# Optimization experiments

Measured on AMD Instinct MI355X. Metric: run time of the kernel, lower is better.

Reference implementation:

```python
import jax, jax.numpy as jnp
import numpy as np

H = 4   # num_attention_heads
C = 32  # attention_head_size
LN_EPS = 1e-5

def setup_inputs() -> dict:
    key = jax.random.key(0)
    ks = jax.random.split(key, 8)
    E = 128  # embedding_channels; all_head_size = H*C = 128
    B, I, J = 1, 256, 256
    s = 1.0 / np.sqrt(E)
    return {
        "z": jax.random.normal(ks[0], (B, I, J, E), dtype=jnp.float32),
        "ln_scale": jnp.ones((E,), jnp.float32),
        "ln_bias": jnp.zeros((E,), jnp.float32),
        # weights stored as [in, out] (torch Linear applies x @ W.T; here y = x @ W)
        "Wq": jax.random.normal(ks[1], (E, H * C), jnp.float32) * s,
        "Wk": jax.random.normal(ks[2], (E, H * C), jnp.float32) * s,
        "Wv": jax.random.normal(ks[3], (E, H * C), jnp.float32) * s,
        "Wg": jax.random.normal(ks[4], (E, H * C), jnp.float32) * s,
        "bg": jnp.zeros((H * C,), jnp.float32),
        "Wo": jax.random.normal(ks[5], (H * C, E), jnp.float32) * s,
        "bo": jnp.zeros((E,), jnp.float32),
    }

def reference(z, ln_scale, ln_bias, Wq, Wk, Wv, Wg, bg, Wo, bo):
    B, I, J, E = z.shape
    # LayerNorm over last dim
    mu = jnp.mean(z, axis=-1, keepdims=True)
    var = jnp.mean(jnp.square(z - mu), axis=-1, keepdims=True)
    zn = (z - mu) * jax.lax.rsqrt(var + LN_EPS) * ln_scale + ln_bias
    # QKV projections, reshaped to heads: [B, I, J, H, C]
    q = (zn @ Wq).reshape(B, I, J, H, C)
    k = (zn @ Wk).reshape(B, I, J, H, C)
    v = (zn @ Wv).reshape(B, I, J, H, C)
    # Row-wise attention (NOTE: original has no 1/sqrt(c) scaling)
    logits = jnp.einsum('biqhc,bikhc->bihqk', q, k)  # [B, I, H, J, J]
    weights = jax.nn.softmax(logits, axis=-1)
    wavg = jnp.einsum('bihqk,bikhc->biqhc', weights, v)  # [B, I, J, H, C]
    # Sigmoid gate
    g = jax.nn.sigmoid((zn @ Wg + bg).reshape(B, I, J, H, C))
    out = (g * wavg).reshape(B, I, J, H * C)
    return out @ Wo + bo
```

## Files before the change

### kernel.cpp

```cpp
#include <hip/hip_runtime.h>

typedef unsigned short u16;
typedef unsigned int   u32;
using bf16x8 = __attribute__((ext_vector_type(8))) __bf16;
using f32x4  = __attribute__((ext_vector_type(4))) float;

#define MFMA16(a,b,c) __builtin_amdgcn_mfma_f32_16x16x32_bf16(a,b,c,0,0,0)

__device__ __forceinline__ float b2f(u16 u){ u32 x = ((u32)u) << 16; return __builtin_bit_cast(float, x); }
__device__ __forceinline__ u16 f2b(float f){
    u32 x = __builtin_bit_cast(u32, f);
    return (u16)((x + 0x7fffu + ((x >> 16) & 1u)) >> 16);
}
__device__ __forceinline__ u32 pk2(float a, float b){ return (u32)f2b(a) | ((u32)f2b(b) << 16); }

constexpr int LDB = 136;
constexpr int LDK = 40;
constexpr int LDV = 264;
constexpr int LDQ = 40;
constexpr int LDZ = 136;

__global__ __launch_bounds__(256) void kw_prep(
    const float* __restrict__ Wq, const float* __restrict__ Wk,
    const float* __restrict__ Wv, const float* __restrict__ Wg,
    const float* __restrict__ Wo, u16* __restrict__ Wt)
{
    const int m = blockIdx.x >> 4;
    const int r = ((blockIdx.x & 15) << 8) | threadIdx.x;
    const int o  = r >> 5;
    const int e4 = (r & 31) << 2;
    const float* __restrict__ src;
    bool lo = false;
    switch (m) {
        case 0: src = Wq; break;
        case 1: src = Wk; break;
        case 2: src = Wv; break;
        case 3: src = Wg; break;
        case 4: src = Wq; lo = true; break;
        case 5: src = Wk; lo = true; break;
        default: src = Wo; break;
    }
    float w[4];
    #pragma unroll
    for (int i = 0; i < 4; ++i) w[i] = src[(e4 + i) * 128 + o];
    if (lo) {
        #pragma unroll
        for (int i = 0; i < 4; ++i) w[i] -= b2f(f2b(w[i]));
    }
    uint2 outv;
    outv.x = pk2(w[0], w[1]);
    outv.y = pk2(w[2], w[3]);
    *(uint2*)(Wt + m * 16384 + o * 128 + e4) = outv;
}

__global__ __launch_bounds__(512, 2) void k1_proj(
    const float* __restrict__ z, const float* __restrict__ lns, const float* __restrict__ lnb,
    const u16* __restrict__ Wt, const float* __restrict__ bg,
    u16* __restrict__ Qo, u16* __restrict__ Ko, u16* __restrict__ Vo, u16* __restrict__ Go)
{
    __shared__ __attribute__((aligned(16))) u16 bufA[128 * LDB];
    __shared__ __attribute__((aligned(16))) u16 bufB[128 * LDB];

    const int t = threadIdx.x;
    const int lane = t & 63;
    const int l15  = lane & 15;
    const int quad = lane >> 4;
    const int wave = t >> 6;
    const int rowbase = blockIdx.x * 128 + wave * 16;
    u16* __restrict__ lntile = bufA + wave * 16 * LDZ;

    bf16x8 zfh[4], zfl[4];
    {
        float sc[32], bi[32];
        #pragma unroll
        for (int u = 0; u < 8; ++u) {
            float4 s4 = *(const float4*)(lns + quad * 32 + u * 4);
            float4 b4 = *(const float4*)(lnb + quad * 32 + u * 4);
            sc[u*4+0]=s4.x; sc[u*4+1]=s4.y; sc[u*4+2]=s4.z; sc[u*4+3]=s4.w;
            bi[u*4+0]=b4.x; bi[u*4+1]=b4.y; bi[u*4+2]=b4.z; bi[u*4+3]=b4.w;
        }
        const size_t tok = (size_t)(rowbase + l15);
        float x[32];
        #pragma unroll
        for (int u = 0; u < 8; ++u) {
            float4 v4 = *(const float4*)(z + (tok << 7) + quad * 32 + u * 4);
            x[u*4+0]=v4.x; x[u*4+1]=v4.y; x[u*4+2]=v4.z; x[u*4+3]=v4.w;
        }
        float s = 0.f;
        #pragma unroll
        for (int k = 0; k < 32; ++k) s += x[k];
        s += __shfl_xor(s, 16, 64); s += __shfl_xor(s, 32, 64);
        const float mu = s * 0.0078125f;
        float vs = 0.f;
        #pragma unroll
        for (int k = 0; k < 32; ++k) { float d = x[k] - mu; vs += d * d; }
        vs += __shfl_xor(vs, 16, 64); vs += __shfl_xor(vs, 32, 64);
        const float rs = rsqrtf(vs * 0.0078125f + 1e-5f);
        float y[32];
        #pragma unroll
        for (int k = 0; k < 32; ++k) y[k] = (x[k] - mu) * rs * sc[k] + bi[k];
        #pragma unroll
        for (int u = 0; u < 4; ++u) {
            uint4 o;
            o.x = pk2(y[u*8+0], y[u*8+1]); o.y = pk2(y[u*8+2], y[u*8+3]);
            o.z = pk2(y[u*8+4], y[u*8+5]); o.w = pk2(y[u*8+6], y[u*8+7]);
            *(uint4*)(lntile + l15 * LDZ + quad * 32 + u * 8) = o;
        }
        #pragma unroll
        for (int ks = 0; ks < 4; ++ks)
            zfh[ks] = *(const bf16x8*)(lntile + l15 * LDZ + ks * 32 + quad * 8);
        #pragma unroll
        for (int k = 0; k < 32; ++k) y[k] -= b2f(f2b(y[k]));
        #pragma unroll
        for (int u = 0; u < 4; ++u) {
            uint4 o;
            o.x = pk2(y[u*8+0], y[u*8+1]); o.y = pk2(y[u*8+2], y[u*8+3]);
            o.z = pk2(y[u*8+4], y[u*8+5]); o.w = pk2(y[u*8+6], y[u*8+7]);
            *(uint4*)(lntile + l15 * LDZ + quad * 32 + u * 8) = o;
        }
        #pragma unroll
        for (int ks = 0; ks < 4; ++ks)
            zfl[ks] = *(const bf16x8*)(lntile + l15 * LDZ + ks * 32 + quad * 8);
    }

    auto stage = [&](u16* __restrict__ buf, const u16* __restrict__ src) {
        #pragma unroll
        for (int u = 0; u < 4; ++u) {
            const int c = (t + u * 512) * 8;
            *(uint4*)(buf + (c >> 7) * LDB + (c & 127)) = *(const uint4*)(src + c);
        }
    };

    u16* Os[4] = {Qo, Ko, Vo, Go};

    #pragma unroll 1
    for (int g = 0; g < 4; ++g) {
        __syncthreads();
        stage(bufA, Wt + g * 16384);
        const bool three = (g < 2);
        if (three) stage(bufB, Wt + (4 + g) * 16384);
        __syncthreads();
        u16* __restrict__ O = Os[g];
        #pragma unroll
        for (int nt = 0; nt < 8; ++nt) {
            f32x4 ac = {0.f, 0.f, 0.f, 0.f};
            const int bbase = (nt * 16 + l15) * LDB + quad * 8;
            #pragma unroll
            for (int ks = 0; ks < 4; ++ks) {
                bf16x8 bh = *(const bf16x8*)(bufA + bbase + ks * 32);
                ac = MFMA16(zfh[ks], bh, ac);
                if (three) {
                    bf16x8 bl = *(const bf16x8*)(bufB + bbase + ks * 32);
                    ac = MFMA16(zfl[ks], bh, ac);
                    ac = MFMA16(zfh[ks], bl, ac);
                }
            }
            const int col = nt * 16 + l15;
            #pragma unroll
            for (int r = 0; r < 4; ++r) {
                float v = ac[r];
                if (g == 3) v = 1.f / (1.f + __expf(-(v + bg[col])));
                O[((size_t)(rowbase + quad * 4 + r) << 7) + col] = f2b(v);
            }
        }
    }
}

__global__ __launch_bounds__(512, 2) void k2_attn(
    u16* QG, const u16* __restrict__ K, const u16* __restrict__ V,
    const u16* __restrict__ G)
{
    __shared__ __attribute__((aligned(16))) u16 kh[256 * 64];
    __shared__ __attribute__((aligned(16))) u16 vt[64 * LDV];
    __shared__ __attribute__((aligned(16))) u16 ptt[8 * 16 * LDQ];

    const int bid = blockIdx.x;
    const int i = bid >> 1, hp = bid & 1;
    const int t = threadIdx.x;
    const int lane = t & 63;
    const int l15  = lane & 15;
    const int quad = lane >> 4;
    const int wave = t >> 6;
    u16* __restrict__ myT = ptt + wave * 16 * LDQ;
    const size_t rb = ((size_t)i) << 8;
    const int cb = hp * 64;

    {
        const int tok = t >> 1, half = t & 1;
        const int swz = (tok & 7) << 3;
        const u16* ksrc = K + ((rb + tok) << 7) + cb + half * 32;
        #pragma unroll
        for (int u = 0; u < 4; ++u)
            *(uint4*)(kh + tok * 64 + ((half * 32 + u * 8) ^ swz)) = *(const uint4*)(ksrc + u * 8);
        const u16* vsrc = V + ((rb + tok) << 7) + cb + half * 32;
        #pragma unroll
        for (int u = 0; u < 4; ++u) {
            uint4 q = *(const uint4*)(vsrc + u * 8);
            u32 w4[4] = {q.x, q.y, q.z, q.w};
            #pragma unroll
            for (int k2 = 0; k2 < 4; ++k2) {
                vt[(half * 32 + u * 8 + k2 * 2    ) * LDV + tok] = (u16)(w4[k2] & 0xffffu);
                vt[(half * 32 + u * 8 + k2 * 2 + 1) * LDV + tok] = (u16)(w4[k2] >> 16);
            }
        }
    }
    __syncthreads();

    #pragma unroll 1
    for (int hh = 0; hh < 2; ++hh) {
        const int hc = cb + hh * 32;
        bf16x8 aq[2];
        f32x4  ga[2][2];
        #pragma unroll
        for (int it = 0; it < 2; ++it) {
            aq[it] = *(const bf16x8*)(QG + ((rb + wave * 32 + it * 16 + l15) << 7) + hc + quad * 8);
            #pragma unroll
            for (int nt = 0; nt < 2; ++nt)
                #pragma unroll
                for (int r = 0; r < 4; ++r)
                    ga[it][nt][r] = b2f(G[((rb + wave * 32 + it * 16 + quad * 4 + r) << 7) + hc + nt * 16 + l15]);
        }

        #pragma unroll 1
        for (int it = 0; it < 2; ++it) {
            f32x4 s[16];
            #pragma unroll
            for (int nt = 0; nt < 16; ++nt) {
                const int key = nt * 16 + l15;
                bf16x8 b = *(const bf16x8*)(kh + key * 64 + ((hh * 32 + quad * 8) ^ ((key & 7) << 3)));
                f32x4 zacc = {0.f, 0.f, 0.f, 0.f};
                s[nt] = MFMA16(aq[it], b, zacc);
            }
            float inv[4];
            #pragma unroll
            for (int r = 0; r < 4; ++r) {
                float mx = s[0][r];
                #pragma unroll
                for (int nt = 1; nt < 16; ++nt) mx = fmaxf(mx, s[nt][r]);
                #pragma unroll
                for (int m = 1; m < 16; m <<= 1) mx = fmaxf(mx, __shfl_xor(mx, m, 64));
                float sm = 0.f;
                #pragma unroll
                for (int nt = 0; nt < 16; ++nt) {
                    float e = __expf(s[nt][r] - mx);
                    s[nt][r] = e; sm += e;
                }
                #pragma unroll
                for (int m = 1; m < 16; m <<= 1) sm += __shfl_xor(sm, m, 64);
                inv[r] = 1.f / sm;
            }
            f32x4 o0 = {0.f,0.f,0.f,0.f}, o1 = {0.f,0.f,0.f,0.f};
            #pragma unroll
            for (int c8 = 0; c8 < 8; ++c8) {
                #pragma unroll
                for (int n2 = 0; n2 < 2; ++n2)
                    #pragma unroll
                    for (int r = 0; r < 4; ++r)
                        myT[(quad * 4 + r) * LDQ + n2 * 16 + l15] = f2b(s[c8 * 2 + n2][r]);
                bf16x8 a  = *(const bf16x8*)(myT + l15 * LDQ + quad * 8);
                bf16x8 b0 = *(const bf16x8*)(vt + (hh * 32 +      l15) * LDV + c8 * 32 + quad * 8);
                bf16x8 b1 = *(const bf16x8*)(vt + (hh * 32 + 16 + l15) * LDV + c8 * 32 + quad * 8);
                o0 = MFMA16(a, b0, o0);
                o1 = MFMA16(a, b1, o1);
            }
            #pragma unroll
            for (int r = 0; r < 4; ++r) {
                u16* dst = QG + ((rb + wave * 32 + it * 16 + quad * 4 + r) << 7) + hc;
                dst[l15]      = f2b(o0[r] * inv[r] * ga[it][0][r]);
                dst[16 + l15] = f2b(o1[r] * inv[r] * ga[it][1][r]);
            }
        }
    }
}

__global__ __launch_bounds__(256, 4) void k3_out(
    const u16* __restrict__ GW, const u16* __restrict__ WoT,
    const float* __restrict__ bo, float* __restrict__ out)
{
    __shared__ __attribute__((aligned(16))) u16 wt[128 * LDB];
    const int t = threadIdx.x;
    const int lane = t & 63;
    const int l15  = lane & 15;
    const int quad = lane >> 4;
    const int wave = t >> 6;
    const int rowbase = blockIdx.x * 64 + wave * 16;

    #pragma unroll
    for (int u = 0; u < 8; ++u) {
        const int c = (t + u * 256) * 8;
        *(uint4*)(wt + (c >> 7) * LDB + (c & 127)) = *(const uint4*)(WoT + c);
    }
    bf16x8 af[4];
    #pragma unroll
    for (int ks = 0; ks < 4; ++ks)
        af[ks] = *(const bf16x8*)(GW + ((size_t)(rowbase + l15) << 7) + ks * 32 + quad * 8);
    __syncthreads();

    #pragma unroll
    for (int nt = 0; nt < 8; ++nt) {
        f32x4 ac = {0.f, 0.f, 0.f, 0.f};
        const int bbase = (nt * 16 + l15) * LDB + quad * 8;
        #pragma unroll
        for (int ks = 0; ks < 4; ++ks) {
            bf16x8 b = *(const bf16x8*)(wt + bbase + ks * 32);
            ac = MFMA16(af[ks], b, ac);
        }
        const int col = nt * 16 + l15;
        const float bb = bo[col];
        #pragma unroll
        for (int r = 0; r < 4; ++r)
            out[((size_t)(rowbase + quad * 4 + r) << 7) + col] = ac[r] + bb;
    }
}

constexpr int FLDZ = 136;
constexpr int FLDW = 136;
constexpr int FLDO = 40;

__global__ __launch_bounds__(512, 2) void k_fused(
    const float* __restrict__ z, const float* __restrict__ lns, const float* __restrict__ lnb,
    const float* __restrict__ Wq, const float* __restrict__ Wk, const float* __restrict__ Wv,
    const float* __restrict__ Wg, const float* __restrict__ bg,
    const float* __restrict__ Wo, const float* __restrict__ bo,
    float* __restrict__ out)
{
    __shared__ __attribute__((aligned(16))) u16 smem[33280];
    const int i = blockIdx.x;
    const int t = threadIdx.x;
    const int lane = t & 63;
    const int l15  = lane & 15;
    const int quad = lane >> 4;
    const int wave = t >> 6;
    u16* __restrict__ kh   = smem;
    u16* __restrict__ vt   = smem + 10240;
    u16* __restrict__ bufA = smem + 18688;
    u16* __restrict__ myT  = smem + 23808 + wave * 16 * LDQ;
    u16* __restrict__ bufB = smem + 28928;
    u16* __restrict__ lntile = smem + wave * 16 * FLDZ;

    float4 wregA[2], wregB[2];
    auto prefW = [&](const float* __restrict__ W, int h, float4 (&r)[2]) {
        #pragma unroll
        for (int k2 = 0; k2 < 2; ++k2) {
            const int c = t * 4 + k2 * 2048;
            r[k2] = *(const float4*)(W + (c >> 5) * 128 + h * 32 + (c & 31));
        }
    };
    auto prefWoF = [&](int h, float4 (&r)[2]) {
        #pragma unroll
        for (int k2 = 0; k2 < 2; ++k2)
            r[k2] = *(const float4*)(Wo + h * 4096 + t * 4 + k2 * 2048);
    };
    auto stageHi = [&](u16* __restrict__ buf, const float4 (&r)[2]) {
        #pragma unroll
        for (int k2 = 0; k2 < 2; ++k2) {
            const int c = t * 4 + k2 * 2048;
            const int e = c >> 5, o = c & 31;
            buf[(o    ) * FLDW + e] = f2b(r[k2].x);
            buf[(o + 1) * FLDW + e] = f2b(r[k2].y);
            buf[(o + 2) * FLDW + e] = f2b(r[k2].z);
            buf[(o + 3) * FLDW + e] = f2b(r[k2].w);
        }
    };
    auto stageLo = [&](u16* __restrict__ buf, const float4 (&r)[2]) {
        #pragma unroll
        for (int k2 = 0; k2 < 2; ++k2) {
            const int c = t * 4 + k2 * 2048;
            const int e = c >> 5, o = c & 31;
            const float v0 = r[k2].x, v1 = r[k2].y, v2 = r[k2].z, v3 = r[k2].w;
            buf[(o    ) * FLDW + e] = f2b(v0 - b2f(f2b(v0)));
            buf[(o + 1) * FLDW + e] = f2b(v1 - b2f(f2b(v1)));
            buf[(o + 2) * FLDW + e] = f2b(v2 - b2f(f2b(v2)));
            buf[(o + 3) * FLDW + e] = f2b(v3 - b2f(f2b(v3)));
        }
    };
    auto stageWoL = [&](const float4 (&r)[2]) {
        #pragma unroll
        for (int k2 = 0; k2 < 2; ++k2) {
            const int c = t * 4 + k2 * 2048;
            const int kk = c >> 7, n = c & 127;
            bufA[(n    ) * FLDO + kk] = f2b(r[k2].x);
            bufA[(n + 1) * FLDO + kk] = f2b(r[k2].y);
            bufA[(n + 2) * FLDO + kk] = f2b(r[k2].z);
            bufA[(n + 3) * FLDO + kk] = f2b(r[k2].w);
        }
    };
    prefW(Wq, 0, wregA);
    bf16x8 zfh[2][4], zfl[2][4];
    {
        float sc[32], bi[32];
        #pragma unroll
        for (int u = 0; u < 8; ++u) {
            float4 s4 = *(const float4*)(lns + quad * 32 + u * 4);
            float4 b4 = *(const float4*)(lnb + quad * 32 + u * 4);
            sc[u*4+0]=s4.x; sc[u*4+1]=s4.y; sc[u*4+2]=s4.z; sc[u*4+3]=s4.w;
            bi[u*4+0]=b4.x; bi[u*4+1]=b4.y; bi[u*4+2]=b4.z; bi[u*4+3]=b4.w;
        }
        #pragma unroll 1
        for (int ms = 0; ms < 2; ++ms) {
            const size_t tok = (size_t)(i * 256 + wave * 32 + ms * 16 + l15);
            float x[32];
            #pragma unroll
            for (int u = 0; u < 8; ++u) {
                float4 v4 = *(const float4*)(z + (tok << 7) + quad * 32 + u * 4);
                x[u*4+0]=v4.x; x[u*4+1]=v4.y; x[u*4+2]=v4.z; x[u*4+3]=v4.w;
            }
            float s = 0.f;
            #pragma unroll
            for (int k = 0; k < 32; ++k) s += x[k];
            s += __shfl_xor(s, 16, 64); s += __shfl_xor(s, 32, 64);
            const float mu = s * 0.0078125f;
            float vs = 0.f;
            #pragma unroll
            for (int k = 0; k < 32; ++k) { float d = x[k] - mu; vs += d * d; }
            vs += __shfl_xor(vs, 16, 64); vs += __shfl_xor(vs, 32, 64);
            const float rs = rsqrtf(vs * 0.0078125f + 1e-5f);
            float y[32];
            #pragma unroll
            for (int k = 0; k < 32; ++k) y[k] = (x[k] - mu) * rs * sc[k] + bi[k];
            #pragma unroll
            for (int u = 0; u < 4; ++u) {
                uint4 o;
                o.x = pk2(y[u*8+0], y[u*8+1]); o.y = pk2(y[u*8+2], y[u*8+3]);
                o.z = pk2(y[u*8+4], y[u*8+5]); o.w = pk2(y[u*8+6], y[u*8+7]);
                *(uint4*)(lntile + l15 * FLDZ + quad * 32 + u * 8) = o;
            }
            #pragma unroll
            for (int ks = 0; ks < 4; ++ks)
                zfh[ms][ks] = *(const bf16x8*)(lntile + l15 * FLDZ + ks * 32 + quad * 8);
            #pragma unroll
            for (int k = 0; k < 32; ++k) y[k] -= b2f(f2b(y[k]));
            #pragma unroll
            for (int u = 0; u < 4; ++u) {
                uint4 o;
                o.x = pk2(y[u*8+0], y[u*8+1]); o.y = pk2(y[u*8+2], y[u*8+3]);
                o.z = pk2(y[u*8+4], y[u*8+5]); o.w = pk2(y[u*8+6], y[u*8+7]);
                *(uint4*)(lntile + l15 * FLDZ + quad * 32 + u * 8) = o;
            }
            #pragma unroll
            for (int ks = 0; ks < 4; ++ks)
                zfl[ms][ks] = *(const bf16x8*)(lntile + l15 * FLDZ + ks * 32 + quad * 8);
        }
    }
    __syncthreads();
    auto gemmAcc = [&](f32x4 (&acc)[2][2], bf16x8 (&af)[2][4], const u16* __restrict__ buf) {
        #pragma unroll
        for (int ms = 0; ms < 2; ++ms)
            #pragma unroll
            for (int nt = 0; nt < 2; ++nt) {
                f32x4 ac = acc[ms][nt];
                #pragma unroll
                for (int ks = 0; ks < 4; ++ks) {
                    bf16x8 b = *(const bf16x8*)(buf + (nt * 16 + l15) * FLDW + ks * 32 + quad * 8);
                    ac = MFMA16(af[ms][ks], b, ac);
                }
                acc[ms][nt] = ac;
            }
    };
    auto zero22 = [](f32x4 (&a)[2][2]) {
        #pragma unroll
        for (int ms = 0; ms < 2; ++ms)
            #pragma unroll
            for (int nt = 0; nt < 2; ++nt) a[ms][nt] = f32x4{0.f,0.f,0.f,0.f};
    };
    bf16x8 aq[2];
    f32x4  ga[2][2];
    f32x4  oacc[2][8];
    #pragma unroll
    for (int ms = 0; ms < 2; ++ms)
        #pragma unroll
        for (int nt = 0; nt < 8; ++nt)
            oacc[ms][nt] = f32x4{0.f, 0.f, 0.f, 0.f};
    #pragma unroll 1
    for (int h = 0; h < 4; ++h) {
        stageHi(bufA, wregA); stageLo(bufB, wregA);
        __syncthreads();
        prefW(Wk, h, wregA);
        {
            f32x4 qa[2][2]; zero22(qa);
            gemmAcc(qa, zfh, bufA); gemmAcc(qa, zfl, bufA); gemmAcc(qa, zfh, bufB);
            #pragma unroll
            for (int ms = 0; ms < 2; ++ms) {
                #pragma unroll
                for (int nt = 0; nt < 2; ++nt)
                    #pragma unroll
                    for (int r = 0; r < 4; ++r)
                        myT[(quad * 4 + r) * LDQ + nt * 16 + l15] = f2b(qa[ms][nt][r]);
                aq[ms] = *(const bf16x8*)(myT + l15 * LDQ + quad * 8);
            }
        }
        __syncthreads();
        stageHi(bufA, wregA); stageLo(bufB, wregA);
        __syncthreads();
        prefW(Wv, h, wregA); prefW(Wg, h, wregB);
        {
            f32x4 ka[2][2]; zero22(ka);
            gemmAcc(ka, zfh, bufA); gemmAcc(ka, zfl, bufA); gemmAcc(ka, zfh, bufB);
            #pragma unroll
            for (int ms = 0; ms < 2; ++ms)
                #pragma unroll
                for (int nt = 0; nt < 2; ++nt)
                    #pragma unroll
                    for (int r = 0; r < 4; ++r)
                        kh[(wave * 32 + ms * 16 + quad * 4 + r) * LDK + nt * 16 + l15] = f2b(ka[ms][nt][r]);
        }
        __syncthreads();
        stageHi(bufA, wregA); stageHi(bufB, wregB);
        __syncthreads();
        prefWoF(h, wregA);
        {
            f32x4 va[2][2]; zero22(va); gemmAcc(va, zfh, bufA);
            #pragma unroll
            for (int ms = 0; ms < 2; ++ms)
                #pragma unroll
                for (int nt = 0; nt < 2; ++nt)
                    #pragma unroll
                    for (int r = 0; r < 4; ++r)
                        vt[(nt * 16 + l15) * LDV + wave * 32 + ms * 16 + quad * 4 + r] = f2b(va[ms][nt][r]);
            zero22(ga); gemmAcc(ga, zfh, bufB);
            #pragma unroll
            for (int nt = 0; nt < 2; ++nt) {
                const float bb = bg[h * 32 + nt * 16 + l15];
                #pragma unroll
                for (int ms = 0; ms < 2; ++ms)
                    #pragma unroll
                    for (int r = 0; r < 4; ++r)
                        ga[ms][nt][r] = 1.f / (1.f + __expf(-(ga[ms][nt][r] + bb)));
            }
        }
        __syncthreads();
        stageWoL(wregA);
        __syncthreads();
        if (h < 3) prefW(Wq, h + 1, wregA);
        #pragma unroll 1
        for (int it = 0; it < 2; ++it) {
            f32x4 s[16];
            #pragma unroll
            for (int nt = 0; nt < 16; ++nt) {
                bf16x8 b = *(const bf16x8*)(kh + (nt * 16 + l15) * LDK + quad * 8);
                f32x4 zacc = {0.f, 0.f, 0.f, 0.f};
                s[nt] = MFMA16(aq[it], b, zacc);
            }
            float inv[4];
            #pragma unroll
            for (int r = 0; r < 4; ++r) {
                float mx = s[0][r];
                #pragma unroll
                for (int nt = 1; nt < 16; ++nt) mx = fmaxf(mx, s[nt][r]);
                #pragma unroll
                for (int m = 1; m < 16; m <<= 1) mx = fmaxf(mx, __shfl_xor(mx, m, 64));
                float sm = 0.f;
                #pragma unroll
                for (int nt = 0; nt < 16; ++nt) {
                    float e = __expf(s[nt][r] - mx);
                    s[nt][r] = e; sm += e;
                }
                #pragma unroll
                for (int m = 1; m < 16; m <<= 1) sm += __shfl_xor(sm, m, 64);
                inv[r] = 1.f / sm;
            }
            f32x4 o0 = {0.f,0.f,0.f,0.f}, o1 = {0.f,0.f,0.f,0.f};
            #pragma unroll
            for (int c8 = 0; c8 < 8; ++c8) {
                #pragma unroll
                for (int n2 = 0; n2 < 2; ++n2)
                    #pragma unroll
                    for (int r = 0; r < 4; ++r)
                        myT[(quad * 4 + r) * LDQ + n2 * 16 + l15] = f2b(s[c8 * 2 + n2][r]);
                bf16x8 a  = *(const bf16x8*)(myT + l15 * LDQ + quad * 8);
                bf16x8 b0 = *(const bf16x8*)(vt + (     l15) * LDV + c8 * 32 + quad * 8);
                bf16x8 b1 = *(const bf16x8*)(vt + (16 + l15) * LDV + c8 * 32 + quad * 8);
                o0 = MFMA16(a, b0, o0);
                o1 = MFMA16(a, b1, o1);
            }
            #pragma unroll
            for (int r = 0; r < 4; ++r) {
                myT[(quad * 4 + r) * LDQ + l15]      = f2b(o0[r] * inv[r] * ga[it][0][r]);
                myT[(quad * 4 + r) * LDQ + 16 + l15] = f2b(o1[r] * inv[r] * ga[it][1][r]);
            }
            bf16x8 agw = *(const bf16x8*)(myT + l15 * LDQ + quad * 8);
            #pragma unroll
            for (int nt = 0; nt < 8; ++nt) {
                bf16x8 bwo = *(const bf16x8*)(bufA + (nt * 16 + l15) * FLDO + quad * 8);
                oacc[it][nt] = MFMA16(agw, bwo, oacc[it][nt]);
            }
        }
        __syncthreads();
    }
    #pragma unroll
    for (int ms = 0; ms < 2; ++ms) {
        #pragma unroll
        for (int nt = 0; nt < 8; ++nt) {
            const int col = nt * 16 + l15;
            const float bb = bo[col];
            #pragma unroll
            for (int r = 0; r < 4; ++r) {
                const size_t row = (size_t)(i * 256 + wave * 32 + ms * 16 + quad * 4 + r);
                out[(row << 7) + col] = oacc[ms][nt][r] + bb;
            }
        }
    }
}

extern "C" void kernel_launch(void* const* d_in, const int* in_sizes, int n_in,
                              void* d_out, int out_size, void* d_ws, size_t ws_size,
                              hipStream_t stream)
{
    const float* z   = (const float*)d_in[0];
    const float* lns = (const float*)d_in[1];
    const float* lnb = (const float*)d_in[2];
    const float* Wq  = (const float*)d_in[3];
    const float* Wk  = (const float*)d_in[4];
    const float* Wv  = (const float*)d_in[5];
    const float* Wg  = (const float*)d_in[6];
    const float* bg  = (const float*)d_in[7];
    const float* Wo  = (const float*)d_in[8];
    const float* bo  = (const float*)d_in[9];
    float* out = (float*)d_out;

    const size_t NEED = 4ull * 65536 * 128 * 2 + 7ull * 16384 * 2;
    if (ws_size >= NEED) {
        u16* Qb = (u16*)d_ws;
        u16* Kb = Qb + 65536ull * 128;
        u16* Vb = Kb + 65536ull * 128;
        u16* Gb = Vb + 65536ull * 128;
        u16* Wt = Gb + 65536ull * 128;
        kw_prep<<<112, 256, 0, stream>>>(Wq, Wk, Wv, Wg, Wo, Wt);
        k1_proj<<<512, 512, 0, stream>>>(z, lns, lnb, Wt, bg, Qb, Kb, Vb, Gb);
        k2_attn<<<512, 512, 0, stream>>>(Qb, Kb, Vb, Gb);
        k3_out<<<1024, 256, 0, stream>>>(Qb, Wt + 6 * 16384, bo, out);
    } else {
        k_fused<<<256, 512, 0, stream>>>(z, lns, lnb, Wq, Wk, Wv, Wg, bg, Wo, bo, out);
    }
}
```

Before: 181.6 us.

## Move sigmoid gate multiply from attention kernel into output projection kernel

The attention kernel no longer loads the gate tensor. It writes the unscaled normalized attention output, batching the two head halves per row group into one set of stores. The output projection kernel now loads the gate alongside the attention output and multiplies them before the MFMA. The attention kernel's launch bounds are raised to 4 blocks per CU to increase occupancy. The gated product is now rounded to bf16 twice instead of once, and the extra gate read is shifted into the final GEMM.

```diff
diff --git a/kernel.cpp b/kernel.cpp
--- a/kernel.cpp
+++ b/kernel.cpp
@@ -166,9 +166,8 @@
     }
 }
 
-__global__ __launch_bounds__(512, 2) void k2_attn(
-    u16* QG, const u16* __restrict__ K, const u16* __restrict__ V,
-    const u16* __restrict__ G)
+__global__ __launch_bounds__(512, 4) void k2_attn(
+    u16* QG, const u16* __restrict__ K, const u16* __restrict__ V)
 {
     __shared__ __attribute__((aligned(16))) u16 kh[256 * 64];
     __shared__ __attribute__((aligned(16))) u16 vt[64 * LDV];
@@ -207,29 +206,20 @@
     __syncthreads();
 
     #pragma unroll 1
-    for (int hh = 0; hh < 2; ++hh) {
-        const int hc = cb + hh * 32;
-        bf16x8 aq[2];
-        f32x4  ga[2][2];
-        #pragma unroll
-        for (int it = 0; it < 2; ++it) {
-            aq[it] = *(const bf16x8*)(QG + ((rb + wave * 32 + it * 16 + l15) << 7) + hc + quad * 8);
-            #pragma unroll
-            for (int nt = 0; nt < 2; ++nt)
-                #pragma unroll
-                for (int r = 0; r < 4; ++r)
-                    ga[it][nt][r] = b2f(G[((rb + wave * 32 + it * 16 + quad * 4 + r) << 7) + hc + nt * 16 + l15]);
-        }
-
-        #pragma unroll 1
-        for (int it = 0; it < 2; ++it) {
+    for (int it = 0; it < 2; ++it) {
+        u32 gwlo[2][4], gwhi[2][4];
+        #pragma unroll
+        for (int hh = 0; hh < 2; ++hh) {
+            const int hc = cb + hh * 32;
+            bf16x8 aq = *(const bf16x8*)(QG + ((rb + wave * 32 + it * 16 + l15) << 7) + hc + quad * 8);
+
             f32x4 s[16];
             #pragma unroll
             for (int nt = 0; nt < 16; ++nt) {
                 const int key = nt * 16 + l15;
                 bf16x8 b = *(const bf16x8*)(kh + key * 64 + ((hh * 32 + quad * 8) ^ ((key & 7) << 3)));
                 f32x4 zacc = {0.f, 0.f, 0.f, 0.f};
-                s[nt] = MFMA16(aq[it], b, zacc);
+                s[nt] = MFMA16(aq, b, zacc);
             }
             float inv[4];
             #pragma unroll
@@ -265,17 +255,25 @@
             }
             #pragma unroll
             for (int r = 0; r < 4; ++r) {
-                u16* dst = QG + ((rb + wave * 32 + it * 16 + quad * 4 + r) << 7) + hc;
-                dst[l15]      = f2b(o0[r] * inv[r] * ga[it][0][r]);
-                dst[16 + l15] = f2b(o1[r] * inv[r] * ga[it][1][r]);
-            }
+                gwlo[hh][r] = f2b(o0[r] * inv[r]);
+                gwhi[hh][r] = f2b(o1[r] * inv[r]);
+            }
+        }
+        #pragma unroll
+        for (int r = 0; r < 4; ++r) {
+            u16* dst = QG + ((rb + wave * 32 + it * 16 + quad * 4 + r) << 7) + cb;
+            dst[     l15] = (u16)gwlo[0][r];
+            dst[16 + l15] = (u16)gwhi[0][r];
+            dst[32 + l15] = (u16)gwlo[1][r];
+            dst[48 + l15] = (u16)gwhi[1][r];
         }
     }
 }
 
 __global__ __launch_bounds__(256, 4) void k3_out(
-    const u16* __restrict__ GW, const u16* __restrict__ WoT,
-    const float* __restrict__ bo, float* __restrict__ out)
+    const u16* __restrict__ GW, const u16* __restrict__ Gb,
+    const u16* __restrict__ WoT, const float* __restrict__ bo,
+    float* __restrict__ out)
 {
     __shared__ __attribute__((aligned(16))) u16 wt[128 * LDB];
     const int t = threadIdx.x;
@@ -291,9 +289,24 @@
         *(uint4*)(wt + (c >> 7) * LDB + (c & 127)) = *(const uint4*)(WoT + c);
     }
     bf16x8 af[4];
-    #pragma unroll
-    for (int ks = 0; ks < 4; ++ks)
-        af[ks] = *(const bf16x8*)(GW + ((size_t)(rowbase + l15) << 7) + ks * 32 + quad * 8);
+    {
+        const size_t rowoff = (size_t)(rowbase + l15) << 7;
+        #pragma unroll
+        for (int ks = 0; ks < 4; ++ks) {
+            bf16x8 a = *(const bf16x8*)(GW + rowoff + ks * 32 + quad * 8);
+            bf16x8 g = *(const bf16x8*)(Gb + rowoff + ks * 32 + quad * 8);
+            const u32* au = (const u32*)&a;
+            const u32* gu = (const u32*)&g;
+            u32 w[4];
+            #pragma unroll
+            for (int j = 0; j < 4; ++j) {
+                float lo = b2f((u16)(au[j] & 0xffffu)) * b2f((u16)(gu[j] & 0xffffu));
+                float hi = b2f((u16)(au[j] >> 16))     * b2f((u16)(gu[j] >> 16));
+                w[j] = pk2(lo, hi);
+            }
+            af[ks] = *(const bf16x8*)w;
+        }
+    }
     __syncthreads();
 
     #pragma unroll
@@ -627,8 +640,8 @@
         u16* Wt = Gb + 65536ull * 128;
         kw_prep<<<112, 256, 0, stream>>>(Wq, Wk, Wv, Wg, Wo, Wt);
         k1_proj<<<512, 512, 0, stream>>>(z, lns, lnb, Wt, bg, Qb, Kb, Vb, Gb);
-        k2_attn<<<512, 512, 0, stream>>>(Qb, Kb, Vb, Gb);
-        k3_out<<<1024, 256, 0, stream>>>(Qb, Wt + 6 * 16384, bo, out);
+        k2_attn<<<512, 512, 0, stream>>>(Qb, Kb, Vb);
+        k3_out<<<1024, 256, 0, stream>>>(Qb, Gb, Wt + 6 * 16384, bo, out);
     } else {
         k_fused<<<256, 512, 0, stream>>>(z, lns, lnb, Wq, Wk, Wv, Wg, bg, Wo, bo, out);
     }
```

Result: faster. 168.3 us (-7.3%).
